# Optimization experiments

Hardware: AMD Instinct MI355X
Metric: run time of the kernel (lower is better)

## Reference

```python
import jax, jax.numpy as jnp
import numpy as np
import math

EMBED_DIM = 512
NUM_HEADS = 8
HEAD_DIM = EMBED_DIM // NUM_HEADS
B, S = 4, 2048


def setup_inputs() -> dict:
    key = jax.random.key(0)
    ks = jax.random.split(key, 12)
    d = EMBED_DIM
    # Xavier-uniform bound for square linear layers
    bound = math.sqrt(6.0 / (d + d))
    def lin_w(k):
        return jax.random.uniform(k, (d, d), jnp.float32, -bound, bound)
    return {
        "x": jax.random.normal(ks[0], (B, S, d), jnp.float32),
        "mask": jax.random.randint(ks[1], (B, S), 0, 2) == 1,  # True = masked out
        "wq": lin_w(ks[2]), "bq": jnp.zeros((d,), jnp.float32),
        "wk": lin_w(ks[3]), "bk": jnp.zeros((d,), jnp.float32),
        "wv": lin_w(ks[4]), "bv": jnp.zeros((d,), jnp.float32),
        "wo": lin_w(ks[5]), "bo": jnp.zeros((d,), jnp.float32),
        "ln_gamma": jnp.ones((d,), jnp.float32),
        "ln_beta": jnp.zeros((d,), jnp.float32),
        "temperature": jnp.full((1,), 1.0 / math.sqrt(HEAD_DIM), jnp.float32),
    }


def _layer_norm(x, gamma, beta, eps=1e-6):
    mu = jnp.mean(x, axis=-1, keepdims=True)
    var = jnp.var(x, axis=-1, keepdims=True)
    return (x - mu) * jax.lax.rsqrt(var + eps) * gamma + beta


def reference(x, mask, wq, bq, wk, bk, wv, bv, wo, bo, ln_gamma, ln_beta, temperature):
    Bv, Sv, d = x.shape
    H, hd = NUM_HEADS, HEAD_DIM
    # torch nn.Linear: y = x @ W.T + b (W is [out, in])
    def proj(w, b):
        return (jnp.einsum("bsd,ed->bse", x, w) + b).reshape(Bv, Sv, H, hd).transpose(0, 2, 1, 3)
    q = proj(wq, bq)  # [B, H, S, hd]
    k = proj(wk, bk)
    v = proj(wv, bv)
    scores = jnp.einsum("bhqd,bhkd->bhqk", q, k) * temperature[0]  # [B,H,S,S]
    scores = jnp.where(mask[:, None, None, :], jnp.float32(-1e9), scores)
    attn = jax.nn.softmax(scores, axis=-1)  # dropout is identity in eval
    out = jnp.einsum("bhqk,bhkd->bhqd", attn, v)
    out = out.transpose(0, 2, 1, 3).reshape(Bv, Sv, d)
    out = jnp.einsum("bsd,ed->bse", out, wo) + bo
    return _layer_norm(out + x, ln_gamma, ln_beta)
```

## Files before the change

kernel.cpp:

```cpp
#include <hip/hip_runtime.h>
#include <hip/hip_bf16.h>
#include <stdint.h>

#define B_ 4
#define S_ 2048
#define D_ 512
#define H_ 8
#define HD_ 64
#define M_ (B_*S_)

typedef __bf16 bf16x8 __attribute__((ext_vector_type(8)));
typedef float f32x4 __attribute__((ext_vector_type(4)));
typedef float f32x16 __attribute__((ext_vector_type(16)));

__device__ __forceinline__ unsigned short f2b(float f) {
  union { float f; unsigned u; } v; v.f = f;
  unsigned r = v.u + 0x7fff + ((v.u >> 16) & 1);
  return (unsigned short)(r >> 16);
}

__device__ __forceinline__ float exp2_hw(float x) {
  return __builtin_amdgcn_exp2f(x);
}

__device__ __forceinline__ unsigned cvtpk_bf16(float lo, float hi) {
  unsigned r;
  asm("v_cvt_pk_bf16_f32 %0, %1, %2" : "=v"(r) : "v"(lo), "v"(hi));
  return r;
}

__device__ __forceinline__ void plswap(unsigned &a, unsigned &b) {
  asm volatile("v_permlane32_swap_b32 %0, %1" : "+v"(a), "+v"(b));
}

__device__ __forceinline__ void gload16(const void* g, void* lds) {
  __builtin_amdgcn_global_load_lds(
      (const __attribute__((address_space(1))) unsigned int*)g,
      (__attribute__((address_space(3))) unsigned int*)lds, 16, 0, 0);
}

#define XN4 (M_ * D_ / 4)
#define WN4 (D_ * D_ / 4)
__global__ __launch_bounds__(256) void cvt_all_kernel(const float* __restrict__ x,
    const float* __restrict__ wq, const float* __restrict__ wk,
    const float* __restrict__ wv, const float* __restrict__ wo,
    unsigned short* __restrict__ xb, unsigned short* __restrict__ wqb,
    unsigned short* __restrict__ wkb, unsigned short* __restrict__ wvb,
    unsigned short* __restrict__ wob) {
  int i = blockIdx.x * blockDim.x + threadIdx.x;
  const float* src; unsigned short* dst; int off;
  if (i < XN4) { src = x; dst = xb; off = i; }
  else {
    int j = i - XN4;
    int sel = j / WN4; off = j - sel * WN4;
    src = (sel == 0) ? wq : (sel == 1) ? wk : (sel == 2) ? wv : wo;
    dst = (sel == 0) ? wqb : (sel == 1) ? wkb : (sel == 2) ? wvb : wob;
  }
  float4 v = ((const float4*)src)[off];
  ushort4 o;
  o.x = f2b(v.x); o.y = f2b(v.y); o.z = f2b(v.z); o.w = f2b(v.w);
  ((ushort4*)dst)[off] = o;
}

__device__ __forceinline__ void gemm_core_db(const unsigned short* __restrict__ A,
                                             const unsigned short* __restrict__ W,
                                             int m0, int n0, f32x4 (&acc)[4][4],
                                             unsigned short (&As)[2][128 * 64],
                                             unsigned short (&Bs)[2][128 * 64]) {
  int tid = threadIdx.x;
  int w = tid >> 6, lane = tid & 63;
  int l15 = lane & 15, g = lane >> 4;
  int wr = w >> 1, wc = w & 1;
  #define STAGE_G(buf, k0_) do {                                               \
    _Pragma("unroll")                                                          \
    for (int i = 0; i < 4; ++i) {                                              \
      int l = i * 256 + w * 64 + lane;                                         \
      int row = l >> 3, seg = l & 7;                                           \
      int sseg = seg ^ (row & 7);                                              \
      gload16(A + (size_t)(m0 + row) * D_ + (k0_) + sseg * 8,                  \
              (char*)As[buf] + (size_t)(i * 256 + w * 64) * 16);               \
      gload16(W + (size_t)(n0 + row) * D_ + (k0_) + sseg * 8,                  \
              (char*)Bs[buf] + (size_t)(i * 256 + w * 64) * 16);               \
    }                                                                          \
  } while (0)
  STAGE_G(0, 0);
  __syncthreads();
  for (int ks = 0; ks < 8; ++ks) {
    int cur = ks & 1;
    if (ks < 7) STAGE_G(cur ^ 1, (ks + 1) * 64);
    #pragma unroll
    for (int kk = 0; kk < 2; ++kk) {
      int sw = ((kk * 4 + g) ^ (l15 & 7)) * 8;
      bf16x8 af[4], bfr[4];
      #pragma unroll
      for (int t = 0; t < 4; ++t) {
        af[t]  = *(const bf16x8*)&As[cur][(wr * 64 + t * 16 + l15) * 64 + sw];
        bfr[t] = *(const bf16x8*)&Bs[cur][(wc * 64 + t * 16 + l15) * 64 + sw];
      }
      #pragma unroll
      for (int mi = 0; mi < 4; ++mi)
        #pragma unroll
        for (int ni = 0; ni < 4; ++ni)
          acc[mi][ni] = __builtin_amdgcn_mfma_f32_16x16x32_bf16(af[mi], bfr[ni], acc[mi][ni], 0, 0, 0);
    }
    __syncthreads();
  }
  #undef STAGE_G
}

__global__ __launch_bounds__(256) void gemm_qkv(const unsigned short* __restrict__ xb,
    const unsigned short* __restrict__ wqb, const unsigned short* __restrict__ wkb,
    const unsigned short* __restrict__ wvb,
    const float* __restrict__ bq, const float* __restrict__ bk, const float* __restrict__ bv,
    const float* __restrict__ tptr,
    unsigned short* __restrict__ Qb, unsigned short* __restrict__ Kb, unsigned short* __restrict__ Vtb) {
  __shared__ unsigned short As[2][128 * 64], Bs[2][128 * 64];
  int z = blockIdx.z;
  const unsigned short* W = (z == 0) ? wqb : ((z == 1) ? wkb : wvb);
  const float* bias = (z == 0) ? bq : ((z == 1) ? bk : bv);
  float scale = (z == 0) ? tptr[0] * 1.44269504088896340736f : 1.0f;
  int m0 = blockIdx.x * 128, n0 = blockIdx.y * 128;
  f32x4 zero4 = {0.f, 0.f, 0.f, 0.f};
  f32x4 acc[4][4];
  #pragma unroll
  for (int mi = 0; mi < 4; ++mi)
    #pragma unroll
    for (int ni = 0; ni < 4; ++ni) acc[mi][ni] = zero4;
  gemm_core_db(xb, W, m0, n0, acc, As, Bs);
  int tid = threadIdx.x;
  int w = tid >> 6, lane = tid & 63, l15 = lane & 15, g = lane >> 4;
  int wr = w >> 1, wc = w & 1;
  if (z == 2) {
    unsigned short* T = &As[0][0];
    #pragma unroll
    for (int mi = 0; mi < 4; ++mi)
      #pragma unroll
      for (int ni = 0; ni < 4; ++ni) {
        int el = wc * 64 + ni * 16 + l15;
        float bb = bias[n0 + el];
        int sx = (el & 15) << 3;
        #pragma unroll
        for (int r = 0; r < 4; ++r) {
          int s = wr * 64 + mi * 16 + g * 4 + r;
          T[el * 128 + (s ^ sx)] = f2b(acc[mi][ni][r] + bb);
        }
      }
    __syncthreads();
    int el = tid >> 1, hf = tid & 1;
    int eg = n0 + el, h = eg >> 6, dd = eg & 63;
    int bI = m0 >> 11, sbase = (m0 & 2047) + hf * 64;
    unsigned short* dst = &Vtb[((size_t)(bI * H_ + h) * HD_ + dd) * S_ + sbase];
    const unsigned short* srcR = &T[el * 128];
    int j = el & 15;
    #pragma unroll
    for (int c = 0; c < 8; ++c) {
      int cc = (hf * 8 + c) ^ j;
      uint4 v = *(const uint4*)&srcR[cc * 8];
      *(uint4*)&dst[c * 8] = v;
    }
  } else {
    #pragma unroll
    for (int mi = 0; mi < 4; ++mi)
      #pragma unroll
      for (int ni = 0; ni < 4; ++ni) {
        int e = n0 + wc * 64 + ni * 16 + l15;
        float bb = bias[e];
        int h = e >> 6, dd = e & 63;
        #pragma unroll
        for (int r = 0; r < 4; ++r) {
          int m = m0 + wr * 64 + mi * 16 + g * 4 + r;
          int b = m >> 11, s = m & 2047;
          unsigned short u = f2b((acc[mi][ni][r] + bb) * scale);
          int bh = b * H_ + h;
          if (z == 0) Qb[((size_t)bh * S_ + s) * HD_ + dd] = u;
          else        Kb[((size_t)bh * S_ + s) * HD_ + dd] = u;
        }
      }
  }
}

__global__ __launch_bounds__(256) void gemm_proj(const unsigned short* __restrict__ AOb,
    const unsigned short* __restrict__ wob, const float* __restrict__ bo, float* __restrict__ Pf) {
  __shared__ unsigned short As[2][128 * 64], Bs[2][128 * 64];
  int m0 = blockIdx.x * 128, n0 = blockIdx.y * 128;
  f32x4 zero4 = {0.f, 0.f, 0.f, 0.f};
  f32x4 acc[4][4];
  #pragma unroll
  for (int mi = 0; mi < 4; ++mi)
    #pragma unroll
    for (int ni = 0; ni < 4; ++ni) acc[mi][ni] = zero4;
  gemm_core_db(AOb, wob, m0, n0, acc, As, Bs);
  int tid = threadIdx.x;
  int w = tid >> 6, lane = tid & 63, l15 = lane & 15, g = lane >> 4;
  int wr = w >> 1, wc = w & 1;
  #pragma unroll
  for (int mi = 0; mi < 4; ++mi)
    #pragma unroll
    for (int ni = 0; ni < 4; ++ni) {
      int e = n0 + wc * 64 + ni * 16 + l15;
      float bb = bo[e];
      #pragma unroll
      for (int r = 0; r < 4; ++r) {
        int m = m0 + wr * 64 + mi * 16 + g * 4 + r;
        Pf[(size_t)m * D_ + e] = acc[mi][ni][r] + bb;
      }
    }
}

__global__ __launch_bounds__(256, 2) void attn_kernel(const unsigned short* __restrict__ Qb,
    const unsigned short* __restrict__ Kb, const unsigned short* __restrict__ Vtb,
    const int* __restrict__ mask, unsigned short* __restrict__ AOb) {
  __shared__ unsigned short Ks[3][64 * 64], Vs[3][64 * 64];
  __shared__ uint4 mlds[32][4][2];
  int bh = blockIdx.y, b = bh >> 3, h = bh & 7;
  int tid = threadIdx.x, w = tid >> 6, lane = tid & 63;
  int l31 = lane & 31, hi = lane >> 5;
  int q0w = blockIdx.x * 128 + w * 32;
  const unsigned short* Qbase = Qb + (size_t)bh * S_ * HD_;
  const int* mbase = mask + (size_t)b * S_;

  bf16x8 qf[4];
  #pragma unroll
  for (int kk = 0; kk < 4; ++kk)
    qf[kk] = *(const bf16x8*)&Qbase[(size_t)(q0w + l31) * HD_ + kk * 16 + hi * 8];

  bf16x8 ones;
  #pragma unroll
  for (int j = 0; j < 8; ++j) ones[j] = (__bf16)1.0f;

  f32x16 out[2], lacc, zc;
  #pragma unroll
  for (int i = 0; i < 16; ++i) { out[0][i] = 0.f; out[1][i] = 0.f; lacc[i] = 0.f; zc[i] = 0.f; }

  f32x16 stA[2], stB[2];

  #define STAGE_KV(buf, kb_) do {                                              \
    _Pragma("unroll")                                                          \
    for (int i = 0; i < 2; ++i) {                                              \
      int l = i * 256 + w * 64 + lane;                                         \
      int row = l >> 3, seg = l & 7;                                           \
      int sseg = seg ^ (row & 7);                                              \
      gload16(Kb + ((size_t)bh * S_ + (kb_) + row) * HD_ + sseg * 8,           \
              (char*)Ks[buf] + (size_t)(i * 256 + w * 64) * 16);               \
      gload16(Vtb + ((size_t)bh * HD_ + row) * S_ + (kb_) + sseg * 8,          \
              (char*)Vs[buf] + (size_t)(i * 256 + w * 64) * 16);               \
    }                                                                          \
  } while (0)

  #define QKT_TILE(KSBUF, ST) do {                                             \
    __builtin_amdgcn_s_setprio(1);                                             \
    const unsigned short* kbase_ = Ks[KSBUF];                                  \
    _Pragma("unroll")                                                          \
    for (int kk = 0; kk < 4; ++kk) {                                           \
      int sw = ((2 * kk + hi) ^ (l31 & 7)) * 8;                                \
      bf16x8 ka0 = *(const bf16x8*)&kbase_[l31 * 64 + sw];                     \
      bf16x8 ka1 = *(const bf16x8*)&kbase_[(32 + l31) * 64 + sw];              \
      ST[0] = __builtin_amdgcn_mfma_f32_32x32x16_bf16(ka0, qf[kk], kk ? ST[0] : zc, 0, 0, 0); \
      ST[1] = __builtin_amdgcn_mfma_f32_32x32x16_bf16(ka1, qf[kk], kk ? ST[1] : zc, 0, 0, 0); \
    }                                                                          \
    __builtin_amdgcn_s_setprio(0);                                             \
  } while (0)

  #define TILE_BODY(T, STC, STN, bPV, bQK, bST) do {                           \
    __syncthreads();                                                           \
    if ((T) + 2 < 32) STAGE_KV(bST, ((T) + 2) * 64);                           \
    if ((T) + 1 < 32) QKT_TILE(bQK, STN);                                      \
    _Pragma("unroll")                                                          \
    for (int ktile = 0; ktile < 2; ++ktile)                                    \
      _Pragma("unroll")                                                        \
      for (int reg = 0; reg < 16; ++reg)                                       \
        STC[ktile][reg] = exp2_hw(STC[ktile][reg]);                            \
    __builtin_amdgcn_s_setprio(1);                                             \
    const unsigned short* vbase_ = Vs[bPV];                                    \
    _Pragma("unroll")                                                          \
    for (int kp = 0; kp < 4; ++kp) {                                           \
      const int kt8 = kp >> 1;                                                 \
      const int ro = 8 * (kp & 1);                                             \
      uint4 mw = mlds[(T)][kp][hi];                                            \
      unsigned Xa = cvtpk_bf16(STC[kt8][ro + 0], STC[kt8][ro + 1]);            \
      unsigned Ya = cvtpk_bf16(STC[kt8][ro + 4], STC[kt8][ro + 5]);            \
      unsigned Xb = cvtpk_bf16(STC[kt8][ro + 2], STC[kt8][ro + 3]);            \
      unsigned Yb = cvtpk_bf16(STC[kt8][ro + 6], STC[kt8][ro + 7]);            \
      plswap(Xa, Ya);                                                          \
      plswap(Xb, Yb);                                                          \
      union { unsigned u[4]; bf16x8 v; } pu;                                   \
      pu.u[0] = Xa & mw.x; pu.u[1] = Xb & mw.y;                                \
      pu.u[2] = Ya & mw.z; pu.u[3] = Yb & mw.w;                                \
      bf16x8 pa = pu.v;                                                        \
      _Pragma("unroll")                                                        \
      for (int dn = 0; dn < 2; ++dn) {                                         \
        int row = dn * 32 + l31;                                               \
        bf16x8 vb = *(const bf16x8*)&vbase_[row * 64 + ((2 * kp + hi) ^ (row & 7)) * 8]; \
        out[dn] = __builtin_amdgcn_mfma_f32_32x32x16_bf16(pa, vb, out[dn], 0, 0, 0); \
      }                                                                        \
      lacc = __builtin_amdgcn_mfma_f32_32x32x16_bf16(pa, ones, lacc, 0, 0, 0); \
    }                                                                          \
    __builtin_amdgcn_s_setprio(0);                                             \
  } while (0)

  STAGE_KV(0, 0);
  {
    int t = tid;
    int tile = t >> 3, kp = (t >> 1) & 3, hh = t & 1;
    const int* mp = mbase + tile * 64 + kp * 16 + hh * 8;
    uint4 mw;
    mw.x = (mp[0] ? 0u : 0x0000FFFFu) | (mp[1] ? 0u : 0xFFFF0000u);
    mw.y = (mp[2] ? 0u : 0x0000FFFFu) | (mp[3] ? 0u : 0xFFFF0000u);
    mw.z = (mp[4] ? 0u : 0x0000FFFFu) | (mp[5] ? 0u : 0xFFFF0000u);
    mw.w = (mp[6] ? 0u : 0x0000FFFFu) | (mp[7] ? 0u : 0xFFFF0000u);
    mlds[tile][kp][hh] = mw;
  }
  __syncthreads();
  STAGE_KV(1, 64);
  QKT_TILE(0, stA);

  int b0 = 0, b1 = 1, b2 = 2;
  for (int tp = 0; tp < 16; ++tp) {
    int t = 2 * tp;
    TILE_BODY(t, stA, stB, b0, b1, b2);
    TILE_BODY(t + 1, stB, stA, b1, b2, b0);
    int btmp = b0; b0 = b2; b2 = b1; b1 = btmp;
  }

  #pragma unroll
  for (int reg = 0; reg < 16; ++reg) {
    float inv = 1.f / lacc[reg];
    int q = q0w + (reg & 3) + 8 * (reg >> 2) + 4 * hi;
    #pragma unroll
    for (int dn = 0; dn < 2; ++dn)
      AOb[((size_t)b * S_ + q) * D_ + h * HD_ + dn * 32 + l31] = f2b(out[dn][reg] * inv);
  }
  #undef TILE_BODY
  #undef QKT_TILE
  #undef STAGE_KV
}

__global__ __launch_bounds__(256) void ln_kernel(const float* __restrict__ Pf,
    const float* __restrict__ x, const float* __restrict__ gamma,
    const float* __restrict__ beta, float* __restrict__ out) {
  int row = blockIdx.x * 4 + (threadIdx.x >> 6);
  int lane = threadIdx.x & 63;
  const float* pr = Pf + (size_t)row * D_;
  const float* xr = x + (size_t)row * D_;
  float4 a0 = *(const float4*)(pr + lane * 4);
  float4 a1 = *(const float4*)(pr + 256 + lane * 4);
  float4 b0 = *(const float4*)(xr + lane * 4);
  float4 b1 = *(const float4*)(xr + 256 + lane * 4);
  float y[8] = {a0.x + b0.x, a0.y + b0.y, a0.z + b0.z, a0.w + b0.w,
                a1.x + b1.x, a1.y + b1.y, a1.z + b1.z, a1.w + b1.w};
  float s = 0.f, s2 = 0.f;
  #pragma unroll
  for (int i = 0; i < 8; ++i) { s += y[i]; s2 += y[i] * y[i]; }
  #pragma unroll
  for (int d = 1; d < 64; d <<= 1) { s += __shfl_xor(s, d); s2 += __shfl_xor(s2, d); }
  float mu = s * (1.f / 512.f);
  float var = s2 * (1.f / 512.f) - mu * mu;
  float inv = rsqrtf(fmaxf(var, 0.f) + 1e-6f);
  float4 g0 = *(const float4*)(gamma + lane * 4);
  float4 g1 = *(const float4*)(gamma + 256 + lane * 4);
  float4 e0 = *(const float4*)(beta + lane * 4);
  float4 e1 = *(const float4*)(beta + 256 + lane * 4);
  float* orow = out + (size_t)row * D_;
  float4 o0 = {(y[0] - mu) * inv * g0.x + e0.x, (y[1] - mu) * inv * g0.y + e0.y,
               (y[2] - mu) * inv * g0.z + e0.z, (y[3] - mu) * inv * g0.w + e0.w};
  float4 o1 = {(y[4] - mu) * inv * g1.x + e1.x, (y[5] - mu) * inv * g1.y + e1.y,
               (y[6] - mu) * inv * g1.z + e1.z, (y[7] - mu) * inv * g1.w + e1.w};
  *(float4*)(orow + lane * 4) = o0;
  *(float4*)(orow + 256 + lane * 4) = o1;
}

extern "C" void kernel_launch(void* const* d_in, const int* in_sizes, int n_in,
                              void* d_out, int out_size, void* d_ws, size_t ws_size,
                              hipStream_t stream) {
  const float* x = (const float*)d_in[0];
  const int* mask = (const int*)d_in[1];
  const float* wq = (const float*)d_in[2];
  const float* bq = (const float*)d_in[3];
  const float* wk = (const float*)d_in[4];
  const float* bk = (const float*)d_in[5];
  const float* wv = (const float*)d_in[6];
  const float* bv = (const float*)d_in[7];
  const float* wo = (const float*)d_in[8];
  const float* bo = (const float*)d_in[9];
  const float* gamma = (const float*)d_in[10];
  const float* beta = (const float*)d_in[11];
  const float* temp = (const float*)d_in[12];
  float* out = (float*)d_out;
  char* ws = (char*)d_ws;
  const size_t MB = (size_t)1 << 20;
  unsigned short* xb  = (unsigned short*)(ws);
  unsigned short* wqb = (unsigned short*)(ws + 8 * MB);
  unsigned short* wkb = (unsigned short*)(ws + 8 * MB + 512 * 1024);
  unsigned short* wvb = (unsigned short*)(ws + 9 * MB);
  unsigned short* wob = (unsigned short*)(ws + 9 * MB + 512 * 1024);
  unsigned short* Qb  = (unsigned short*)(ws + 10 * MB);
  unsigned short* Kb  = (unsigned short*)(ws + 18 * MB);
  float*          Pf  = (float*)(ws + 10 * MB);
  unsigned short* Vtb = (unsigned short*)(ws + 26 * MB);
  unsigned short* AOb = (unsigned short*)(ws + 34 * MB);

  cvt_all_kernel<<<(XN4 + 4 * WN4 + 255) / 256, 256, 0, stream>>>(
      x, wq, wk, wv, wo, xb, wqb, wkb, wvb, wob);
  gemm_qkv<<<dim3(64, 4, 3), 256, 0, stream>>>(xb, wqb, wkb, wvb, bq, bk, bv, temp, Qb, Kb, Vtb);
  attn_kernel<<<dim3(16, 32), 256, 0, stream>>>(Qb, Kb, Vtb, mask, AOb);
  gemm_proj<<<dim3(64, 4), 256, 0, stream>>>(AOb, wob, bo, Pf);
  ln_kernel<<<2048, 256, 0, stream>>>(Pf, x, gamma, beta, out);
}
```

Before: 105.2 us.

## Store projection output in bf16 and remap attention blocks per XCD

The output projection now writes its pre-LayerNorm result as bf16 instead of fp32, halving that intermediate's write and read traffic, and LayerNorm converts it back while also switching to a contiguous 8-element-per-lane layout. Attention blocks are remapped so that consecutive block IDs, which the hardware spreads across the eight XCDs, send all query blocks of a given batch-head to the same XCD to improve K/V L2 reuse. Rounding the pre-residual projection to bf16 adds some precision loss.

```diff
diff --git a/kernel.cpp b/kernel.cpp
--- a/kernel.cpp
+++ b/kernel.cpp
@@ -17,6 +17,11 @@
   union { float f; unsigned u; } v; v.f = f;
   unsigned r = v.u + 0x7fff + ((v.u >> 16) & 1);
   return (unsigned short)(r >> 16);
+}
+
+__device__ __forceinline__ float b2f(unsigned short u) {
+  union { unsigned u; float f; } v; v.u = (unsigned)u << 16;
+  return v.f;
 }
 
 __device__ __forceinline__ float exp2_hw(float x) {
@@ -180,7 +185,8 @@
 }
 
 __global__ __launch_bounds__(256) void gemm_proj(const unsigned short* __restrict__ AOb,
-    const unsigned short* __restrict__ wob, const float* __restrict__ bo, float* __restrict__ Pf) {
+    const unsigned short* __restrict__ wob, const float* __restrict__ bo,
+    unsigned short* __restrict__ Pfb) {
   __shared__ unsigned short As[2][128 * 64], Bs[2][128 * 64];
   int m0 = blockIdx.x * 128, n0 = blockIdx.y * 128;
   f32x4 zero4 = {0.f, 0.f, 0.f, 0.f};
@@ -202,7 +208,7 @@
       #pragma unroll
       for (int r = 0; r < 4; ++r) {
         int m = m0 + wr * 64 + mi * 16 + g * 4 + r;
-        Pf[(size_t)m * D_ + e] = acc[mi][ni][r] + bb;
+        Pfb[(size_t)m * D_ + e] = f2b(acc[mi][ni][r] + bb);
       }
     }
 }
@@ -212,10 +218,14 @@
     const int* __restrict__ mask, unsigned short* __restrict__ AOb) {
   __shared__ unsigned short Ks[3][64 * 64], Vs[3][64 * 64];
   __shared__ uint4 mlds[32][4][2];
-  int bh = blockIdx.y, b = bh >> 3, h = bh & 7;
+  int bid = blockIdx.y * gridDim.x + blockIdx.x;
+  int xcd = bid & 7, j = bid >> 3;
+  int bh = xcd * 4 + (j >> 4);
+  int qblk = j & 15;
+  int b = bh >> 3, h = bh & 7;
   int tid = threadIdx.x, w = tid >> 6, lane = tid & 63;
   int l31 = lane & 31, hi = lane >> 5;
-  int q0w = blockIdx.x * 128 + w * 32;
+  int q0w = qblk * 128 + w * 32;
   const unsigned short* Qbase = Qb + (size_t)bh * S_ * HD_;
   const int* mbase = mask + (size_t)b * S_;
 
@@ -226,7 +236,7 @@
 
   bf16x8 ones;
   #pragma unroll
-  for (int j = 0; j < 8; ++j) ones[j] = (__bf16)1.0f;
+  for (int jj = 0; jj < 8; ++jj) ones[jj] = (__bf16)1.0f;
 
   f32x16 out[2], lacc, zc;
   #pragma unroll
@@ -335,19 +345,19 @@
   #undef STAGE_KV
 }
 
-__global__ __launch_bounds__(256) void ln_kernel(const float* __restrict__ Pf,
+__global__ __launch_bounds__(256) void ln_kernel(const unsigned short* __restrict__ Pfb,
     const float* __restrict__ x, const float* __restrict__ gamma,
     const float* __restrict__ beta, float* __restrict__ out) {
   int row = blockIdx.x * 4 + (threadIdx.x >> 6);
   int lane = threadIdx.x & 63;
-  const float* pr = Pf + (size_t)row * D_;
+  const unsigned short* pr = Pfb + (size_t)row * D_;
   const float* xr = x + (size_t)row * D_;
-  float4 a0 = *(const float4*)(pr + lane * 4);
-  float4 a1 = *(const float4*)(pr + 256 + lane * 4);
-  float4 b0 = *(const float4*)(xr + lane * 4);
-  float4 b1 = *(const float4*)(xr + 256 + lane * 4);
-  float y[8] = {a0.x + b0.x, a0.y + b0.y, a0.z + b0.z, a0.w + b0.w,
-                a1.x + b1.x, a1.y + b1.y, a1.z + b1.z, a1.w + b1.w};
+  ushort4 p0 = *(const ushort4*)(pr + lane * 8);
+  ushort4 p1 = *(const ushort4*)(pr + lane * 8 + 4);
+  float4 b0 = *(const float4*)(xr + lane * 8);
+  float4 b1 = *(const float4*)(xr + lane * 8 + 4);
+  float y[8] = {b2f(p0.x) + b0.x, b2f(p0.y) + b0.y, b2f(p0.z) + b0.z, b2f(p0.w) + b0.w,
+                b2f(p1.x) + b1.x, b2f(p1.y) + b1.y, b2f(p1.z) + b1.z, b2f(p1.w) + b1.w};
   float s = 0.f, s2 = 0.f;
   #pragma unroll
   for (int i = 0; i < 8; ++i) { s += y[i]; s2 += y[i] * y[i]; }
@@ -356,17 +366,17 @@
   float mu = s * (1.f / 512.f);
   float var = s2 * (1.f / 512.f) - mu * mu;
   float inv = rsqrtf(fmaxf(var, 0.f) + 1e-6f);
-  float4 g0 = *(const float4*)(gamma + lane * 4);
-  float4 g1 = *(const float4*)(gamma + 256 + lane * 4);
-  float4 e0 = *(const float4*)(beta + lane * 4);
-  float4 e1 = *(const float4*)(beta + 256 + lane * 4);
+  float4 g0 = *(const float4*)(gamma + lane * 8);
+  float4 g1 = *(const float4*)(gamma + lane * 8 + 4);
+  float4 e0 = *(const float4*)(beta + lane * 8);
+  float4 e1 = *(const float4*)(beta + lane * 8 + 4);
   float* orow = out + (size_t)row * D_;
   float4 o0 = {(y[0] - mu) * inv * g0.x + e0.x, (y[1] - mu) * inv * g0.y + e0.y,
                (y[2] - mu) * inv * g0.z + e0.z, (y[3] - mu) * inv * g0.w + e0.w};
   float4 o1 = {(y[4] - mu) * inv * g1.x + e1.x, (y[5] - mu) * inv * g1.y + e1.y,
                (y[6] - mu) * inv * g1.z + e1.z, (y[7] - mu) * inv * g1.w + e1.w};
-  *(float4*)(orow + lane * 4) = o0;
-  *(float4*)(orow + 256 + lane * 4) = o1;
+  *(float4*)(orow + lane * 8) = o0;
+  *(float4*)(orow + lane * 8 + 4) = o1;
 }
 
 extern "C" void kernel_launch(void* const* d_in, const int* in_sizes, int n_in,
@@ -395,7 +405,7 @@
   unsigned short* wob = (unsigned short*)(ws + 9 * MB + 512 * 1024);
   unsigned short* Qb  = (unsigned short*)(ws + 10 * MB);
   unsigned short* Kb  = (unsigned short*)(ws + 18 * MB);
-  float*          Pf  = (float*)(ws + 10 * MB);
+  unsigned short* Pfb = (unsigned short*)(ws + 10 * MB);
   unsigned short* Vtb = (unsigned short*)(ws + 26 * MB);
   unsigned short* AOb = (unsigned short*)(ws + 34 * MB);
 
@@ -403,6 +413,6 @@
       x, wq, wk, wv, wo, xb, wqb, wkb, wvb, wob);
   gemm_qkv<<<dim3(64, 4, 3), 256, 0, stream>>>(xb, wqb, wkb, wvb, bq, bk, bv, temp, Qb, Kb, Vtb);
   attn_kernel<<<dim3(16, 32), 256, 0, stream>>>(Qb, Kb, Vtb, mask, AOb);
-  gemm_proj<<<dim3(64, 4), 256, 0, stream>>>(AOb, wob, bo, Pf);
-  ln_kernel<<<2048, 256, 0, stream>>>(Pf, x, gamma, beta, out);
-}
+  gemm_proj<<<dim3(64, 4), 256, 0, stream>>>(AOb, wob, bo, Pfb);
+  ln_kernel<<<2048, 256, 0, stream>>>(Pfb, x, gamma, beta, out);
+}
```

New measurement: 101.9 us. -3.2%, faster.
